# Performance work log

Hardware: AMD Instinct MI355X
Metric: run time of the kernel (lower is better)

## Reference

```python
import jax, jax.numpy as jnp
import numpy as np

B, S, DM, DH, H, R = 2, 4096, 512, 512, 8, 4
HD = DH // H
SCALING = 1.0 / R  # alpha / r = 1.0 / 4


def setup_inputs() -> dict:
    key = jax.random.key(0)
    ks = jax.random.split(key, 12)
    lim = 1.0 / np.sqrt(DM)  # kaiming_uniform(a=sqrt(5)) bound for fan_in=DM
    inp = {
        "x": jax.random.normal(ks[0], (B, S, DM), dtype=jnp.float32),
        "atten_mask": jax.random.randint(ks[1], (B, S), 0, 2, dtype=jnp.int32),
        "Wk": jax.random.uniform(ks[2], (DH, DM), jnp.float32, -lim, lim),
        "Wq": jax.random.uniform(ks[3], (DH, DM), jnp.float32, -lim, lim),
        "Wv": jax.random.uniform(ks[4], (DH, DM), jnp.float32, -lim, lim),
        "Aq": jax.random.normal(ks[5], (R, DM), dtype=jnp.float32) * 0.01,
        "Bq": jax.random.normal(ks[6], (DH, R), dtype=jnp.float32) * 0.01,
        "Av": jax.random.normal(ks[7], (R, DM), dtype=jnp.float32) * 0.01,
        "Bv": jax.random.normal(ks[8], (DH, R), dtype=jnp.float32) * 0.01,
        "Wp": jax.random.uniform(ks[9], (DM, DH), jnp.float32, -1.0 / np.sqrt(DH), 1.0 / np.sqrt(DH)),
        "bp": jax.random.uniform(ks[10], (DM,), jnp.float32, -1.0 / np.sqrt(DH), 1.0 / np.sqrt(DH)),
    }
    return inp


def _heads(t):
    # [B,S,DH] -> [B,H,S,HD]
    return t.reshape(B, S, H, HD).transpose(0, 2, 1, 3)


def reference(x, atten_mask, Wk, Wq, Wv, Aq, Bq, Av, Bv, Wp, bp):
    k = x @ Wk.T
    q = x @ Wq.T + SCALING * ((x @ Aq.T) @ Bq.T)
    v = x @ Wv.T + SCALING * ((x @ Av.T) @ Bv.T)
    qh, kh, vh = _heads(q), _heads(k), _heads(v)
    scores = jnp.einsum("bhqd,bhkd->bhqk", qh, kh) / jnp.sqrt(jnp.float32(HD))
    neg = jnp.finfo(scores.dtype).min  # acts like -inf fill
    mask = (atten_mask == 0)[:, None, None, :]  # [B,1,1,S] over keys
    scores = jnp.where(mask, -jnp.inf, scores)
    probs = jax.nn.softmax(scores, axis=-1)
    ctx = jnp.einsum("bhqk,bhkd->bhqd", probs, vh)
    ctx = ctx.transpose(0, 2, 1, 3).reshape(B, S, DH)
    return ctx @ Wp.T + bp
```

## Files before the change

### kernel.cpp

```cpp
#include <hip/hip_runtime.h>
#include <hip/hip_bf16.h>
#include <stdint.h>

#define B_   2
#define S_   4096
#define DM_  512
#define DH_  512
#define H_   8
#define BS_  (B_*S_)
#define NX_  (BS_*DM_)
#define NW_  (DM_*DH_)
#define LOG2E 1.4426950408889634f
#define QSCALE (0.125f*LOG2E)

typedef __attribute__((ext_vector_type(4))) float f32x4;
typedef __attribute__((ext_vector_type(4))) short s16x4;
typedef __attribute__((ext_vector_type(8))) short s16x8;

__device__ __forceinline__ short f2bf(float x){
  uint32_t u = __builtin_bit_cast(uint32_t, x);
  u = (u + 0x7fffu + ((u >> 16) & 1u)) >> 16;
  return (short)u;
}
__device__ __forceinline__ float exp2fast(float x){ return __builtin_amdgcn_exp2f(x); }

__global__ __launch_bounds__(256) void conv_kernel(
    const float* __restrict__ x,  const float* __restrict__ Wk,
    const float* __restrict__ Wq, const float* __restrict__ Wv,
    const float* __restrict__ Wp, const int* __restrict__ mask,
    short* __restrict__ xbf,  short* __restrict__ wkbf, short* __restrict__ wqbf,
    short* __restrict__ wvbf, short* __restrict__ wpbf, float* __restrict__ biasw)
{
  const int tid = blockIdx.x*256 + threadIdx.x;
  if (tid < BS_) biasw[tid] = mask[tid] ? 0.f : -1e30f;
  size_t idx = (size_t)tid*8;
  const float* src; short* dst; size_t off;
  if (idx < NX_)                      { src=x;  dst=xbf;  off=idx; }
  else if (idx < NX_+(size_t)NW_)     { src=Wk; dst=wkbf; off=idx-NX_; }
  else if (idx < NX_+2*(size_t)NW_)   { src=Wq; dst=wqbf; off=idx-NX_-NW_; }
  else if (idx < NX_+3*(size_t)NW_)   { src=Wv; dst=wvbf; off=idx-NX_-2*(size_t)NW_; }
  else                                { src=Wp; dst=wpbf; off=idx-NX_-3*(size_t)NW_; }
  f32x4 a = *(const f32x4*)(src+off);
  f32x4 b = *(const f32x4*)(src+off+4);
  s16x8 o;
  o[0]=f2bf(a.x); o[1]=f2bf(a.y); o[2]=f2bf(a.z); o[3]=f2bf(a.w);
  o[4]=f2bf(b.x); o[5]=f2bf(b.y); o[6]=f2bf(b.z); o[7]=f2bf(b.w);
  *(s16x8*)(dst+off) = o;
}

__global__ __launch_bounds__(256) void lorau_kernel(
    const float* __restrict__ x, const float* __restrict__ Aq,
    const float* __restrict__ Av, float* __restrict__ Uq, float* __restrict__ Uv){
  const int lane = threadIdx.x & 63, w = threadIdx.x >> 6;
  const int row = blockIdx.x*4 + w;
  const f32x4* xp = (const f32x4*)(x + (size_t)row*DM_ + lane*8);
  f32x4 x0 = xp[0], x1 = xp[1];
  float acc[8];
  #pragma unroll
  for (int r=0;r<4;r++){
    const f32x4* ap = (const f32x4*)(Aq + r*DM_ + lane*8);
    f32x4 a0 = ap[0], a1 = ap[1];
    const f32x4* vp = (const f32x4*)(Av + r*DM_ + lane*8);
    f32x4 b0 = vp[0], b1 = vp[1];
    acc[r]   = x0.x*a0.x + x0.y*a0.y + x0.z*a0.z + x0.w*a0.w
             + x1.x*a1.x + x1.y*a1.y + x1.z*a1.z + x1.w*a1.w;
    acc[4+r] = x0.x*b0.x + x0.y*b0.y + x0.z*b0.z + x0.w*b0.w
             + x1.x*b1.x + x1.y*b1.y + x1.z*b1.z + x1.w*b1.w;
  }
  #pragma unroll
  for (int i=0;i<8;i++){
    float v = acc[i];
    #pragma unroll
    for (int m=1;m<64;m<<=1) v += __shfl_xor(v, m);
    acc[i] = v;
  }
  if (lane == 0){
    #pragma unroll
    for (int r=0;r<4;r++){ Uq[row*4+r] = acc[r]; Uv[row*4+r] = acc[4+r]; }
  }
}

__global__ __launch_bounds__(256) void qkv_kernel(
    const short* __restrict__ xbf,
    const short* __restrict__ wkbf, const short* __restrict__ wqbf,
    const short* __restrict__ wvbf,
    const float* __restrict__ Uq, const float* __restrict__ Bq,
    const float* __restrict__ Uv, const float* __restrict__ Bv,
    short* __restrict__ kw, short* __restrict__ qw, short* __restrict__ vw)
{
  __shared__ __align__(16) short As[128*32];
  __shared__ __align__(16) short Bsm[64*32];
  const int t = threadIdx.x;
  const int lane = t & 63, w = t >> 6;
  const int g = lane >> 4, l15 = lane & 15;
  const int m0 = blockIdx.x * 128;
  const int proj = blockIdx.y >> 3;
  const int n0 = (blockIdx.y & 7) * 64;
  const short* W = proj==0 ? wkbf : (proj==1 ? wqbf : wvbf);

  f32x4 acc[2][4];
  #pragma unroll
  for (int i=0;i<2;i++)
    #pragma unroll
    for (int j=0;j<4;j++){ f32x4 z = {0.f,0.f,0.f,0.f}; acc[i][j] = z; }

  const int rA0 = t >> 2,        sA0 = t & 3;
  const int rA1 = (t+256) >> 2,  sA1 = t & 3;
  const int rB  = t >> 2,        sB  = t & 3;

  const short* pa0 = xbf + (size_t)(m0+rA0)*DM_ + sA0*8;
  const short* pa1 = xbf + (size_t)(m0+rA1)*DM_ + sA1*8;
  const short* pbp = W   + (size_t)(n0+rB )*DM_ + sB *8;
  short* wa0 = (short*)((char*)As  + rA0*64 + ((sA0 ^ (rA0&3))*16));
  short* wa1 = (short*)((char*)As  + rA1*64 + ((sA1 ^ (rA1&3))*16));
  short* wb  = (short*)((char*)Bsm + rB *64 + ((sB  ^ (rB &3))*16));

  s16x8 va0 = *(const s16x8*)pa0; pa0 += 32;
  s16x8 va1 = *(const s16x8*)pa1; pa1 += 32;
  s16x8 vb  = *(const s16x8*)pbp; pbp += 32;

  for (int kt=0; kt<16; ++kt){
    __syncthreads();
    *(s16x8*)wa0 = va0;
    *(s16x8*)wa1 = va1;
    *(s16x8*)wb  = vb;
    __syncthreads();

    if (kt+1 < 16){
      va0 = *(const s16x8*)pa0; pa0 += 32;
      va1 = *(const s16x8*)pa1; pa1 += 32;
      vb  = *(const s16x8*)pbp; pbp += 32;
    }

    s16x8 af[2], bfr[4];
    #pragma unroll
    for (int mf=0; mf<2; ++mf){
      int rr = w*32 + mf*16 + l15;
      af[mf] = *(const s16x8*)((const char*)As + rr*64 + ((g ^ (rr&3))*16));
    }
    #pragma unroll
    for (int nf=0; nf<4; ++nf){
      int rr = nf*16 + l15;
      bfr[nf] = *(const s16x8*)((const char*)Bsm + rr*64 + ((g ^ (rr&3))*16));
    }
    __builtin_amdgcn_s_setprio(1);
    #pragma unroll
    for (int mf=0; mf<2; ++mf)
      #pragma unroll
      for (int nf=0; nf<4; ++nf)
        acc[mf][nf] = __builtin_amdgcn_mfma_f32_16x16x32_bf16(af[mf], bfr[nf], acc[mf][nf], 0, 0, 0);
    __builtin_amdgcn_s_setprio(0);
  }

  short* outp = proj==0 ? kw : (proj==1 ? qw : vw);
  const float* Um = (proj==1) ? Uq : Uv;
  const float* Bm = (proj==1) ? Bq : Bv;
  #pragma unroll
  for (int mf=0; mf<2; ++mf){
    #pragma unroll
    for (int r=0; r<4; ++r){
      const int m = m0 + w*32 + mf*16 + g*4 + r;
      f32x4 uvec = {0.f,0.f,0.f,0.f};
      if (proj) uvec = *(const f32x4*)(Um + m*4);
      #pragma unroll
      for (int nf=0; nf<4; ++nf){
        const int cn = n0 + nf*16 + l15;
        float val = acc[mf][nf][r];
        if (proj){
          f32x4 bb = *(const f32x4*)(Bm + cn*4);
          val += 0.25f*(uvec.x*bb.x + uvec.y*bb.y + uvec.z*bb.z + uvec.w*bb.w);
        }
        if (proj==1) val *= QSCALE;
        outp[(size_t)m*DH_ + cn] = f2bf(val);
      }
    }
  }
}

__global__ __launch_bounds__(256) void vt_kernel(const short* __restrict__ vw, short* __restrict__ vt){
  __shared__ __align__(16) short T[64*72];
  const int t = threadIdx.x;
  const int st = blockIdx.x, bh = blockIdx.y;
  const int b = bh >> 3, h = bh & 7;
  #pragma unroll
  for (int p=0;p<2;p++){
    int c = t + p*256;
    int row = c >> 3, off = c & 7;
    s16x8 v = *(const s16x8*)(vw + (size_t)(b*S_ + st*64 + row)*DH_ + h*64 + off*8);
    *(s16x8*)((char*)T + row*144 + off*16) = v;
  }
  __syncthreads();
  #pragma unroll
  for (int p=0;p<2;p++){
    int c = t + p*256;
    int d = c >> 3, soff = c & 7;
    s16x8 o;
    #pragma unroll
    for (int j=0;j<8;j++)
      o[j] = *((const short*)((const char*)T + (soff*8+j)*144 + d*2));
    *(s16x8*)(vt + (size_t)(bh*64 + d)*S_ + st*64 + soff*8) = o;
  }
}

__global__ __launch_bounds__(256) void attn_kernel(
    const short* __restrict__ qw, const short* __restrict__ kw,
    const short* __restrict__ vtw, const float* __restrict__ biasw,
    short* __restrict__ ctxw)
{
  __shared__ __align__(16) char smem[24576];
  short* Ks = (short*)smem;
  short* Vs = (short*)(smem + 8192);
  char*  Ps = smem + 16384;
  const int t = threadIdx.x, lane = t & 63, w = t >> 6;
  const int g = lane >> 4, l15 = lane & 15;
  const int bid = blockIdx.x;
  const int xcd = bid & 7, jj = bid >> 3;
  const int bh = xcd*2 + (jj >> 6), qb = jj & 63;
  const int b = bh >> 3, h = bh & 7;
  const int qr0 = qb*64 + w*16;

  s16x8 qf[2];
  #pragma unroll
  for (int ks=0;ks<2;ks++)
    qf[ks] = *(const s16x8*)(qw + (size_t)(b*S_ + qr0 + l15)*DH_ + h*64 + ks*32 + g*8);

  const float* gb = biasw + b*S_ + g*4;
  const short* kbase = kw + (size_t)(b*S_)*DH_ + h*64;
  const short* vbase = vtw + (size_t)(bh*64)*S_;
  char* Pw = Ps + w*2048;

  f32x4 ctx[5];
  #pragma unroll
  for (int n=0;n<5;n++){ f32x4 z = {0.f,0.f,0.f,0.f}; ctx[n] = z; }

  const s16x8 ones = { 0x3F80,0x3F80,0x3F80,0x3F80,0x3F80,0x3F80,0x3F80,0x3F80 };

  const int c1 = t + 256;
  const int r0 = t >> 3,  o0 = t & 7;
  const int r1 = c1 >> 3, o1 = c1 & 7;
  const short* kp0 = kbase + (size_t)r0*DH_ + o0*8;
  const short* kp1 = kbase + (size_t)r1*DH_ + o1*8;
  const short* vp0 = vbase + (size_t)r0*S_ + o0*8;
  const short* vp1 = vbase + (size_t)r1*S_ + o1*8;
  char* wk0 = (char*)Ks + r0*128 + ((o0 ^ (r0&7))*16);
  char* wk1 = (char*)Ks + r1*128 + ((o1 ^ (r1&7))*16);
  char* wv0 = (char*)Vs + r0*128 + ((o0 ^ (r0&7))*16);
  char* wv1 = (char*)Vs + r1*128 + ((o1 ^ (r1&7))*16);

  s16x8 kv0 = *(const s16x8*)kp0; kp0 += 64*DH_;
  s16x8 kv1 = *(const s16x8*)kp1; kp1 += 64*DH_;
  s16x8 vv0 = *(const s16x8*)vp0; vp0 += 64;
  s16x8 vv1 = *(const s16x8*)vp1; vp1 += 64;
  f32x4 bvn[4];
  #pragma unroll
  for (int sb=0; sb<4; ++sb) bvn[sb] = *(const f32x4*)(gb + sb*16);

  for (int kt=0; kt<64; ++kt){
    __syncthreads();
    *(s16x8*)wk0 = kv0; *(s16x8*)wk1 = kv1;
    *(s16x8*)wv0 = vv0; *(s16x8*)wv1 = vv1;
    __syncthreads();

    f32x4 bv[4];
    #pragma unroll
    for (int sb=0; sb<4; ++sb) bv[sb] = bvn[sb];

    if (kt+1 < 64){
      kv0 = *(const s16x8*)kp0; kp0 += 64*DH_;
      kv1 = *(const s16x8*)kp1; kp1 += 64*DH_;
      vv0 = *(const s16x8*)vp0; vp0 += 64;
      vv1 = *(const s16x8*)vp1; vp1 += 64;
      const float* gn = gb + (kt+1)*64;
      #pragma unroll
      for (int sb=0; sb<4; ++sb) bvn[sb] = *(const f32x4*)(gn + sb*16);
    }

    f32x4 st[4];
    __builtin_amdgcn_s_setprio(1);
    #pragma unroll
    for (int sb=0; sb<4; ++sb){
      f32x4 s = bv[sb];
      #pragma unroll
      for (int ks=0; ks<2; ++ks){
        int row = sb*16 + l15;
        s16x8 kf = *(const s16x8*)((const char*)Ks + row*128 + (((ks*4+g) ^ (row&7))*16));
        s = __builtin_amdgcn_mfma_f32_16x16x32_bf16(kf, qf[ks], s, 0, 0, 0);
      }
      st[sb] = s;
    }
    __builtin_amdgcn_s_setprio(0);

    #pragma unroll
    for (int sb=0; sb<4; ++sb){
      union { __hip_bfloat16 h[4]; s16x4 v; } cv;
      cv.h[0] = __float2bfloat16(exp2fast(st[sb][0]));
      cv.h[1] = __float2bfloat16(exp2fast(st[sb][1]));
      cv.h[2] = __float2bfloat16(exp2fast(st[sb][2]));
      cv.h[3] = __float2bfloat16(exp2fast(st[sb][3]));
      int slot = (sb*2 + (g>>1)) ^ (l15 & 7);
      *(s16x4*)(Pw + l15*128 + slot*16 + (g&1)*8) = cv.v;
    }

    __builtin_amdgcn_s_setprio(1);
    #pragma unroll
    for (int ks=0; ks<2; ++ks){
      s16x8 pf = *(const s16x8*)(Pw + l15*128 + (((ks*4+g) ^ (l15&7))*16));
      #pragma unroll
      for (int n=0;n<4;n++){
        int row = n*16 + l15;
        s16x8 vf = *(const s16x8*)((const char*)Vs + row*128 + (((ks*4+g) ^ (row&7))*16));
        ctx[n] = __builtin_amdgcn_mfma_f32_16x16x32_bf16(pf, vf, ctx[n], 0, 0, 0);
      }
      ctx[4] = __builtin_amdgcn_mfma_f32_16x16x32_bf16(pf, ones, ctx[4], 0, 0, 0);
    }
    __builtin_amdgcn_s_setprio(0);
  }

  float inv[4];
  #pragma unroll
  for (int r=0;r<4;r++) inv[r] = 1.f / ctx[4][r];
  #pragma unroll
  for (int n=0;n<4;n++)
    #pragma unroll
    for (int r=0;r<4;r++){
      int m = b*S_ + qr0 + g*4 + r;
      ctxw[(size_t)m*DH_ + h*64 + n*16 + l15] = f2bf(ctx[n][r] * inv[r]);
    }
}

__global__ __launch_bounds__(256) void oproj_kernel(
    const short* __restrict__ ctxw, const short* __restrict__ wpbf,
    const float* __restrict__ bp, float* __restrict__ out)
{
  __shared__ __align__(16) short As[128*32];
  __shared__ __align__(16) short Bsm[64*32];
  const int t = threadIdx.x, lane = t & 63, w = t >> 6;
  const int g = lane >> 4, l15 = lane & 15;
  const int m0 = blockIdx.x*128, n0 = blockIdx.y*64;
  f32x4 acc[2][4];
  #pragma unroll
  for (int i=0;i<2;i++)
    #pragma unroll
    for (int j=0;j<4;j++){ f32x4 z = {0.f,0.f,0.f,0.f}; acc[i][j] = z; }

  const int rA0 = t >> 2,        sA0 = t & 3;
  const int rA1 = (t+256) >> 2,  sA1 = t & 3;
  const int rB  = t >> 2,        sB  = t & 3;

  const short* pa0 = ctxw + (size_t)(m0+rA0)*DH_ + sA0*8;
  const short* pa1 = ctxw + (size_t)(m0+rA1)*DH_ + sA1*8;
  const short* pbp = wpbf + (size_t)(n0+rB )*DH_ + sB *8;
  short* wa0 = (short*)((char*)As  + rA0*64 + ((sA0 ^ (rA0&3))*16));
  short* wa1 = (short*)((char*)As  + rA1*64 + ((sA1 ^ (rA1&3))*16));
  short* wb  = (short*)((char*)Bsm + rB *64 + ((sB  ^ (rB &3))*16));

  s16x8 va0 = *(const s16x8*)pa0; pa0 += 32;
  s16x8 va1 = *(const s16x8*)pa1; pa1 += 32;
  s16x8 vb  = *(const s16x8*)pbp; pbp += 32;

  for (int kt=0; kt<16; ++kt){
    __syncthreads();
    *(s16x8*)wa0 = va0;
    *(s16x8*)wa1 = va1;
    *(s16x8*)wb  = vb;
    __syncthreads();

    if (kt+1 < 16){
      va0 = *(const s16x8*)pa0; pa0 += 32;
      va1 = *(const s16x8*)pa1; pa1 += 32;
      vb  = *(const s16x8*)pbp; pbp += 32;
    }

    s16x8 af[2], bfr[4];
    #pragma unroll
    for (int mf=0; mf<2; ++mf){
      int rr = w*32 + mf*16 + l15;
      af[mf] = *(const s16x8*)((const char*)As + rr*64 + ((g ^ (rr&3))*16));
    }
    #pragma unroll
    for (int nf=0; nf<4; ++nf){
      int rr = nf*16 + l15;
      bfr[nf] = *(const s16x8*)((const char*)Bsm + rr*64 + ((g ^ (rr&3))*16));
    }
    __builtin_amdgcn_s_setprio(1);
    #pragma unroll
    for (int mf=0; mf<2; ++mf)
      #pragma unroll
      for (int nf=0; nf<4; ++nf)
        acc[mf][nf] = __builtin_amdgcn_mfma_f32_16x16x32_bf16(af[mf], bfr[nf], acc[mf][nf], 0, 0, 0);
    __builtin_amdgcn_s_setprio(0);
  }

  #pragma unroll
  for (int mf=0; mf<2; ++mf)
    #pragma unroll
    for (int nf=0; nf<4; ++nf){
      const int cn = n0 + nf*16 + l15;
      const float bpv = bp[cn];
      #pragma unroll
      for (int r=0;r<4;r++){
        const int m = m0 + w*32 + mf*16 + g*4 + r;
        out[(size_t)m*DM_ + cn] = acc[mf][nf][r] + bpv;
      }
    }
}

extern "C" void kernel_launch(void* const* d_in, const int* in_sizes, int n_in,
                              void* d_out, int out_size, void* d_ws, size_t ws_size,
                              hipStream_t stream)
{
  const float* x  = (const float*)d_in[0];
  const int* mask = (const int*)d_in[1];
  const float* Wk = (const float*)d_in[2];
  const float* Wq = (const float*)d_in[3];
  const float* Wv = (const float*)d_in[4];
  const float* Aq = (const float*)d_in[5];
  const float* Bq = (const float*)d_in[6];
  const float* Av = (const float*)d_in[7];
  const float* Bv = (const float*)d_in[8];
  const float* Wp = (const float*)d_in[9];
  const float* bp = (const float*)d_in[10];
  float* out = (float*)d_out;

  char* ws = (char*)d_ws;
  short* qw   = (short*)(ws);
  short* kw   = (short*)(ws + 8388608);
  short* vw   = (short*)(ws + 16777216);
  short* vtw  = (short*)(ws + 25165824);
  short* xbf  = (short*)(ws + 25165824);
  short* ctxw = (short*)(ws + 16777216);
  float* Uq   = (float*)(ws + 33554432);
  float* Uv   = (float*)(ws + 33685504);
  float* biasw= (float*)(ws + 33816576);
  short* wkbf = (short*)(ws + 33849344);
  short* wqbf = (short*)(ws + 34373632);
  short* wvbf = (short*)(ws + 34897920);
  short* wpbf = (short*)(ws + 35422208);

  conv_kernel<<<dim3(2560), dim3(256), 0, stream>>>(x, Wk, Wq, Wv, Wp, mask,
                                                    xbf, wkbf, wqbf, wvbf, wpbf, biasw);
  lorau_kernel<<<dim3(2048), dim3(256), 0, stream>>>(x, Aq, Av, Uq, Uv);
  qkv_kernel<<<dim3(64, 24), dim3(256), 0, stream>>>(xbf, wkbf, wqbf, wvbf,
                                                     Uq, Bq, Uv, Bv, kw, qw, vw);
  vt_kernel<<<dim3(64, 16), dim3(256), 0, stream>>>(vw, vtw);
  attn_kernel<<<dim3(1024), dim3(256), 0, stream>>>(qw, kw, vtw, biasw, ctxw);
  oproj_kernel<<<dim3(64, 8), dim3(256), 0, stream>>>(ctxw, wpbf, bp, out);
  (void)in_sizes; (void)n_in; (void)out_size; (void)ws_size;
}
```

Before: 268.4 us.

## Double query rows per attention wave and merge conversion with LoRA kernel

```diff
diff --git a/kernel.cpp b/kernel.cpp
--- a/kernel.cpp
+++ b/kernel.cpp
@@ -24,59 +24,60 @@
 }
 __device__ __forceinline__ float exp2fast(float x){ return __builtin_amdgcn_exp2f(x); }
 
-__global__ __launch_bounds__(256) void conv_kernel(
+__global__ __launch_bounds__(256) void convlora_kernel(
     const float* __restrict__ x,  const float* __restrict__ Wk,
     const float* __restrict__ Wq, const float* __restrict__ Wv,
     const float* __restrict__ Wp, const int* __restrict__ mask,
+    const float* __restrict__ Aq, const float* __restrict__ Av,
     short* __restrict__ xbf,  short* __restrict__ wkbf, short* __restrict__ wqbf,
-    short* __restrict__ wvbf, short* __restrict__ wpbf, float* __restrict__ biasw)
+    short* __restrict__ wvbf, short* __restrict__ wpbf,
+    float* __restrict__ biasw, float* __restrict__ Uq, float* __restrict__ Uv)
 {
-  const int tid = blockIdx.x*256 + threadIdx.x;
-  if (tid < BS_) biasw[tid] = mask[tid] ? 0.f : -1e30f;
-  size_t idx = (size_t)tid*8;
-  const float* src; short* dst; size_t off;
-  if (idx < NX_)                      { src=x;  dst=xbf;  off=idx; }
-  else if (idx < NX_+(size_t)NW_)     { src=Wk; dst=wkbf; off=idx-NX_; }
-  else if (idx < NX_+2*(size_t)NW_)   { src=Wq; dst=wqbf; off=idx-NX_-NW_; }
-  else if (idx < NX_+3*(size_t)NW_)   { src=Wv; dst=wvbf; off=idx-NX_-2*(size_t)NW_; }
-  else                                { src=Wp; dst=wpbf; off=idx-NX_-3*(size_t)NW_; }
-  f32x4 a = *(const f32x4*)(src+off);
-  f32x4 b = *(const f32x4*)(src+off+4);
-  s16x8 o;
-  o[0]=f2bf(a.x); o[1]=f2bf(a.y); o[2]=f2bf(a.z); o[3]=f2bf(a.w);
-  o[4]=f2bf(b.x); o[5]=f2bf(b.y); o[6]=f2bf(b.z); o[7]=f2bf(b.w);
-  *(s16x8*)(dst+off) = o;
-}
-
-__global__ __launch_bounds__(256) void lorau_kernel(
-    const float* __restrict__ x, const float* __restrict__ Aq,
-    const float* __restrict__ Av, float* __restrict__ Uq, float* __restrict__ Uv){
-  const int lane = threadIdx.x & 63, w = threadIdx.x >> 6;
-  const int row = blockIdx.x*4 + w;
-  const f32x4* xp = (const f32x4*)(x + (size_t)row*DM_ + lane*8);
-  f32x4 x0 = xp[0], x1 = xp[1];
-  float acc[8];
-  #pragma unroll
-  for (int r=0;r<4;r++){
-    const f32x4* ap = (const f32x4*)(Aq + r*DM_ + lane*8);
-    f32x4 a0 = ap[0], a1 = ap[1];
-    const f32x4* vp = (const f32x4*)(Av + r*DM_ + lane*8);
-    f32x4 b0 = vp[0], b1 = vp[1];
-    acc[r]   = x0.x*a0.x + x0.y*a0.y + x0.z*a0.z + x0.w*a0.w
-             + x1.x*a1.x + x1.y*a1.y + x1.z*a1.z + x1.w*a1.w;
-    acc[4+r] = x0.x*b0.x + x0.y*b0.y + x0.z*b0.z + x0.w*b0.w
-             + x1.x*b1.x + x1.y*b1.y + x1.z*b1.z + x1.w*b1.w;
-  }
-  #pragma unroll
-  for (int i=0;i<8;i++){
-    float v = acc[i];
-    #pragma unroll
-    for (int m=1;m<64;m<<=1) v += __shfl_xor(v, m);
-    acc[i] = v;
-  }
-  if (lane == 0){
-    #pragma unroll
-    for (int r=0;r<4;r++){ Uq[row*4+r] = acc[r]; Uv[row*4+r] = acc[4+r]; }
+  const int bid = blockIdx.x;
+  if (bid < 2560){
+    const int tid = bid*256 + threadIdx.x;
+    if (tid < BS_) biasw[tid] = mask[tid] ? 0.f : -1e30f;
+    size_t idx = (size_t)tid*8;
+    const float* src; short* dst; size_t off;
+    if (idx < NX_)                      { src=x;  dst=xbf;  off=idx; }
+    else if (idx < NX_+(size_t)NW_)     { src=Wk; dst=wkbf; off=idx-NX_; }
+    else if (idx < NX_+2*(size_t)NW_)   { src=Wq; dst=wqbf; off=idx-NX_-NW_; }
+    else if (idx < NX_+3*(size_t)NW_)   { src=Wv; dst=wvbf; off=idx-NX_-2*(size_t)NW_; }
+    else                                { src=Wp; dst=wpbf; off=idx-NX_-3*(size_t)NW_; }
+    f32x4 a = *(const f32x4*)(src+off);
+    f32x4 b = *(const f32x4*)(src+off+4);
+    s16x8 o;
+    o[0]=f2bf(a.x); o[1]=f2bf(a.y); o[2]=f2bf(a.z); o[3]=f2bf(a.w);
+    o[4]=f2bf(b.x); o[5]=f2bf(b.y); o[6]=f2bf(b.z); o[7]=f2bf(b.w);
+    *(s16x8*)(dst+off) = o;
+  } else {
+    const int lane = threadIdx.x & 63, w = threadIdx.x >> 6;
+    const int row = (bid-2560)*4 + w;
+    const f32x4* xp = (const f32x4*)(x + (size_t)row*DM_ + lane*8);
+    f32x4 x0 = xp[0], x1 = xp[1];
+    float acc[8];
+    #pragma unroll
+    for (int r=0;r<4;r++){
+      const f32x4* ap = (const f32x4*)(Aq + r*DM_ + lane*8);
+      f32x4 a0 = ap[0], a1 = ap[1];
+      const f32x4* vp = (const f32x4*)(Av + r*DM_ + lane*8);
+      f32x4 b0 = vp[0], b1 = vp[1];
+      acc[r]   = x0.x*a0.x + x0.y*a0.y + x0.z*a0.z + x0.w*a0.w
+               + x1.x*a1.x + x1.y*a1.y + x1.z*a1.z + x1.w*a1.w;
+      acc[4+r] = x0.x*b0.x + x0.y*b0.y + x0.z*b0.z + x0.w*b0.w
+               + x1.x*b1.x + x1.y*b1.y + x1.z*b1.z + x1.w*b1.w;
+    }
+    #pragma unroll
+    for (int i=0;i<8;i++){
+      float v = acc[i];
+      #pragma unroll
+      for (int m=1;m<64;m<<=1) v += __shfl_xor(v, m);
+      acc[i] = v;
+    }
+    if (lane == 0){
+      #pragma unroll
+      for (int r=0;r<4;r++){ Uq[row*4+r] = acc[r]; Uv[row*4+r] = acc[4+r]; }
+    }
   }
 }
 
@@ -207,7 +208,7 @@
     const short* __restrict__ vtw, const float* __restrict__ biasw,
     short* __restrict__ ctxw)
 {
-  __shared__ __align__(16) char smem[24576];
+  __shared__ __align__(16) char smem[32768];
   short* Ks = (short*)smem;
   short* Vs = (short*)(smem + 8192);
   char*  Ps = smem + 16384;
@@ -215,23 +216,28 @@
   const int g = lane >> 4, l15 = lane & 15;
   const int bid = blockIdx.x;
   const int xcd = bid & 7, jj = bid >> 3;
-  const int bh = xcd*2 + (jj >> 6), qb = jj & 63;
+  const int bh = xcd*2 + (jj >> 5), qb = jj & 31;
   const int b = bh >> 3, h = bh & 7;
-  const int qr0 = qb*64 + w*16;
-
-  s16x8 qf[2];
-  #pragma unroll
-  for (int ks=0;ks<2;ks++)
-    qf[ks] = *(const s16x8*)(qw + (size_t)(b*S_ + qr0 + l15)*DH_ + h*64 + ks*32 + g*8);
+  const int qr0 = qb*128 + w*32;
+
+  s16x8 qf[2][2];
+  #pragma unroll
+  for (int tile=0;tile<2;tile++)
+    #pragma unroll
+    for (int ks=0;ks<2;ks++)
+      qf[tile][ks] = *(const s16x8*)(qw + (size_t)(b*S_ + qr0 + tile*16 + l15)*DH_
+                                     + h*64 + ks*32 + g*8);
 
   const float* gb = biasw + b*S_ + g*4;
   const short* kbase = kw + (size_t)(b*S_)*DH_ + h*64;
   const short* vbase = vtw + (size_t)(bh*64)*S_;
-  char* Pw = Ps + w*2048;
-
-  f32x4 ctx[5];
-  #pragma unroll
-  for (int n=0;n<5;n++){ f32x4 z = {0.f,0.f,0.f,0.f}; ctx[n] = z; }
+  char* Pw = Ps + w*4096;
+
+  f32x4 ctx[2][5];
+  #pragma unroll
+  for (int tile=0;tile<2;tile++)
+    #pragma unroll
+    for (int n=0;n<5;n++){ f32x4 z = {0.f,0.f,0.f,0.f}; ctx[tile][n] = z; }
 
   const s16x8 ones = { 0x3F80,0x3F80,0x3F80,0x3F80,0x3F80,0x3F80,0x3F80,0x3F80 };
 
@@ -275,57 +281,71 @@
       for (int sb=0; sb<4; ++sb) bvn[sb] = *(const f32x4*)(gn + sb*16);
     }
 
-    f32x4 st[4];
+    f32x4 stA[4], stB[4];
     __builtin_amdgcn_s_setprio(1);
     #pragma unroll
     for (int sb=0; sb<4; ++sb){
-      f32x4 s = bv[sb];
+      f32x4 sA = bv[sb], sB = bv[sb];
       #pragma unroll
       for (int ks=0; ks<2; ++ks){
         int row = sb*16 + l15;
         s16x8 kf = *(const s16x8*)((const char*)Ks + row*128 + (((ks*4+g) ^ (row&7))*16));
-        s = __builtin_amdgcn_mfma_f32_16x16x32_bf16(kf, qf[ks], s, 0, 0, 0);
+        sA = __builtin_amdgcn_mfma_f32_16x16x32_bf16(kf, qf[0][ks], sA, 0, 0, 0);
+        sB = __builtin_amdgcn_mfma_f32_16x16x32_bf16(kf, qf[1][ks], sB, 0, 0, 0);
       }
-      st[sb] = s;
+      stA[sb] = sA; stB[sb] = sB;
     }
     __builtin_amdgcn_s_setprio(0);
 
     #pragma unroll
     for (int sb=0; sb<4; ++sb){
-      union { __hip_bfloat16 h[4]; s16x4 v; } cv;
-      cv.h[0] = __float2bfloat16(exp2fast(st[sb][0]));
-      cv.h[1] = __float2bfloat16(exp2fast(st[sb][1]));
-      cv.h[2] = __float2bfloat16(exp2fast(st[sb][2]));
-      cv.h[3] = __float2bfloat16(exp2fast(st[sb][3]));
       int slot = (sb*2 + (g>>1)) ^ (l15 & 7);
-      *(s16x4*)(Pw + l15*128 + slot*16 + (g&1)*8) = cv.v;
+      char* base = Pw + l15*128 + slot*16 + (g&1)*8;
+      union { __hip_bfloat16 h[4]; s16x4 v; } cvA, cvB;
+      cvA.h[0] = __float2bfloat16(exp2fast(stA[sb][0]));
+      cvA.h[1] = __float2bfloat16(exp2fast(stA[sb][1]));
+      cvA.h[2] = __float2bfloat16(exp2fast(stA[sb][2]));
+      cvA.h[3] = __float2bfloat16(exp2fast(stA[sb][3]));
+      cvB.h[0] = __float2bfloat16(exp2fast(stB[sb][0]));
+      cvB.h[1] = __float2bfloat16(exp2fast(stB[sb][1]));
+      cvB.h[2] = __float2bfloat16(exp2fast(stB[sb][2]));
+      cvB.h[3] = __float2bfloat16(exp2fast(stB[sb][3]));
+      *(s16x4*)(base)        = cvA.v;
+      *(s16x4*)(base + 2048) = cvB.v;
     }
 
     __builtin_amdgcn_s_setprio(1);
     #pragma unroll
     for (int ks=0; ks<2; ++ks){
-      s16x8 pf = *(const s16x8*)(Pw + l15*128 + (((ks*4+g) ^ (l15&7))*16));
+      const char* pb = Pw + l15*128 + (((ks*4+g) ^ (l15&7))*16);
+      s16x8 pfA = *(const s16x8*)(pb);
+      s16x8 pfB = *(const s16x8*)(pb + 2048);
       #pragma unroll
       for (int n=0;n<4;n++){
         int row = n*16 + l15;
         s16x8 vf = *(const s16x8*)((const char*)Vs + row*128 + (((ks*4+g) ^ (row&7))*16));
-        ctx[n] = __builtin_amdgcn_mfma_f32_16x16x32_bf16(pf, vf, ctx[n], 0, 0, 0);
+        ctx[0][n] = __builtin_amdgcn_mfma_f32_16x16x32_bf16(pfA, vf, ctx[0][n], 0, 0, 0);
+        ctx[1][n] = __builtin_amdgcn_mfma_f32_16x16x32_bf16(pfB, vf, ctx[1][n], 0, 0, 0);
       }
-      ctx[4] = __builtin_amdgcn_mfma_f32_16x16x32_bf16(pf, ones, ctx[4], 0, 0, 0);
+      ctx[0][4] = __builtin_amdgcn_mfma_f32_16x16x32_bf16(pfA, ones, ctx[0][4], 0, 0, 0);
+      ctx[1][4] = __builtin_amdgcn_mfma_f32_16x16x32_bf16(pfB, ones, ctx[1][4], 0, 0, 0);
     }
     __builtin_amdgcn_s_setprio(0);
   }
 
-  float inv[4];
-  #pragma unroll
-  for (int r=0;r<4;r++) inv[r] = 1.f / ctx[4][r];
-  #pragma unroll
-  for (int n=0;n<4;n++)
-    #pragma unroll
-    for (int r=0;r<4;r++){
-      int m = b*S_ + qr0 + g*4 + r;
-      ctxw[(size_t)m*DH_ + h*64 + n*16 + l15] = f2bf(ctx[n][r] * inv[r]);
-    }
+  #pragma unroll
+  for (int tile=0;tile<2;tile++){
+    float inv[4];
+    #pragma unroll
+    for (int r=0;r<4;r++) inv[r] = 1.f / ctx[tile][4][r];
+    #pragma unroll
+    for (int n=0;n<4;n++)
+      #pragma unroll
+      for (int r=0;r<4;r++){
+        int m = b*S_ + qr0 + tile*16 + g*4 + r;
+        ctxw[(size_t)m*DH_ + h*64 + n*16 + l15] = f2bf(ctx[tile][n][r] * inv[r]);
+      }
+  }
 }
 
 __global__ __launch_bounds__(256) void oproj_kernel(
@@ -437,13 +457,13 @@
   short* wvbf = (short*)(ws + 34897920);
   short* wpbf = (short*)(ws + 35422208);
 
-  conv_kernel<<<dim3(2560), dim3(256), 0, stream>>>(x, Wk, Wq, Wv, Wp, mask,
-                                                    xbf, wkbf, wqbf, wvbf, wpbf, biasw);
-  lorau_kernel<<<dim3(2048), dim3(256), 0, stream>>>(x, Aq, Av, Uq, Uv);
+  convlora_kernel<<<dim3(4608), dim3(256), 0, stream>>>(
+      x, Wk, Wq, Wv, Wp, mask, Aq, Av,
+      xbf, wkbf, wqbf, wvbf, wpbf, biasw, Uq, Uv);
   qkv_kernel<<<dim3(64, 24), dim3(256), 0, stream>>>(xbf, wkbf, wqbf, wvbf,
                                                      Uq, Bq, Uv, Bv, kw, qw, vw);
   vt_kernel<<<dim3(64, 16), dim3(256), 0, stream>>>(vw, vtw);
-  attn_kernel<<<dim3(1024), dim3(256), 0, stream>>>(qw, kw, vtw, biasw, ctxw);
+  attn_kernel<<<dim3(512), dim3(256), 0, stream>>>(qw, kw, vtw, biasw, ctxw);
   oproj_kernel<<<dim3(64, 8), dim3(256), 0, stream>>>(ctxw, wpbf, bp, out);
   (void)in_sizes; (void)n_in; (void)out_size; (void)ws_size;
 }
```

After: 240.5 us. 10.4% less time.
